# Optimization experiments

Measured on AMD Instinct MI355X. Metric: run time of the kernel, lower is better.

The kernel has to match this reference:

```python
import jax, jax.numpy as jnp
import numpy as np

N = 50000
E = 800000
F_IN = 128
F_HID = 128
F_OUT = 64


def setup_inputs() -> dict:
    key = jax.random.key(0)
    ks = jax.random.split(key, 16)
    x = jax.random.normal(ks[0], (N, F_IN), dtype=jnp.float32)
    ei1 = jax.random.randint(ks[1], (2, E), 0, N, dtype=jnp.int32)
    ei2 = jax.random.randint(ks[2], (2, E), 0, N, dtype=jnp.int32)
    ei3 = jax.random.randint(ks[3], (2, E), 0, N, dtype=jnp.int32)
    s = lambda k, i, o: jax.random.normal(k, (i, o), dtype=jnp.float32) / np.sqrt(i)
    Wl1 = s(ks[4], F_IN, F_HID); Wr1 = s(ks[5], F_IN, F_HID); b1 = jnp.zeros((F_HID,), jnp.float32)
    Wl2 = s(ks[6], F_HID, F_HID); Wr2 = s(ks[7], F_HID, F_HID); b2 = jnp.zeros((F_HID,), jnp.float32)
    Wl3 = s(ks[8], F_HID, F_OUT); Wr3 = s(ks[9], F_HID, F_OUT); b3 = jnp.zeros((F_OUT,), jnp.float32)
    return {"x": x, "ei1": ei1, "ei2": ei2, "ei3": ei3,
            "Wl1": Wl1, "Wr1": Wr1, "b1": b1,
            "Wl2": Wl2, "Wr2": Wr2, "b2": b2,
            "Wl3": Wl3, "Wr3": Wr3, "b3": b3}


def sage_conv(x, ei, Wl, Wr, b):
    # mean aggregation over incoming edges: src=ei[0] -> dst=ei[1]
    msg = x[ei[0]]                                            # [E, F]
    agg = jax.ops.segment_sum(msg, ei[1], num_segments=N)     # [N, F]
    cnt = jax.ops.segment_sum(jnp.ones((ei.shape[1],), x.dtype), ei[1], num_segments=N)
    mean = agg / jnp.maximum(cnt, 1.0)[:, None]
    # out = lin_l(mean) + lin_r(x_target); full-graph so x_target = x
    return mean @ Wl + b + x @ Wr


def reference(x, ei1, ei2, ei3, Wl1, Wr1, b1, Wl2, Wr2, b2, Wl3, Wr3, b3):
    # in_conv + relu (dropout is identity in eval mode)
    h = jax.nn.relu(sage_conv(x, ei1, Wl1, Wr1, b1))
    # mid_conv + relu + residual skip
    m = jax.nn.relu(sage_conv(h, ei2, Wl2, Wr2, b2))
    h = m + h
    # out_conv (no norm, no activation)
    return sage_conv(h, ei3, Wl3, Wr3, b3)
```

## Files before the change

kernel.cpp:

```cpp
#include <hip/hip_runtime.h>

#define FDIM 128
#define NBMAX 128
#define CAPB 10240

typedef short short8 __attribute__((ext_vector_type(8)));
typedef float f32x4 __attribute__((ext_vector_type(4)));

static __device__ __forceinline__ unsigned short f2bf(float f) {
    unsigned u = __float_as_uint(f);
    u += 0x7FFF + ((u >> 16) & 1);
    return (unsigned short)(u >> 16);
}
static __device__ __forceinline__ float bf2f(unsigned short h) {
    return __uint_as_float(((unsigned)h) << 16);
}

__global__ __launch_bounds__(256) void pack_kernel(
    int* __restrict__ gCnt, int nb3,
    const float* __restrict__ Wl1, const float* __restrict__ Wr1,
    const float* __restrict__ Wl2, const float* __restrict__ Wr2,
    const float* __restrict__ Wl3, const float* __restrict__ Wr3,
    ushort* __restrict__ Wp1, ushort* __restrict__ Wp2, ushort* __restrict__ Wp3)
{
    int b = blockIdx.x;
    if (b == 0) {
        for (int k = threadIdx.x; k < nb3; k += 256) gCnt[k] = 0;
    }
    if (b < 32) {
        const float *Wl, *Wr; ushort* Wp; int base;
        if (b < 16) { Wl = Wl1; Wr = Wr1; Wp = Wp1; base = b; }
        else        { Wl = Wl2; Wr = Wr2; Wp = Wp2; base = b - 16; }
        int idx = base * 256 + threadIdx.x;
        int lane = idx & 63;
        int jt = (idx >> 6) % 8;
        int kt = (idx >> 6) / 8;
        int kbase = kt * 32 + (lane >> 4) * 8;
        int j = jt * 16 + (lane & 15);
        const float* W = (kbase < 128) ? Wl : Wr;
        int kb = kbase & 127;
        ushort tmp[8];
#pragma unroll
        for (int t = 0; t < 8; ++t) tmp[t] = f2bf(W[(size_t)(kb + t) * 128 + j]);
        *reinterpret_cast<uint4*>(Wp + (size_t)idx * 8) = *reinterpret_cast<uint4*>(tmp);
        return;
    }
    int idx = (b - 32) * 256 + threadIdx.x;
    if (idx >= 4 * 8 * 64) return;
    int lane = idx & 63;
    int jt = (idx >> 6) % 8;
    int kt = (idx >> 6) / 8;
    int kbase = kt * 32 + (lane >> 4) * 8;
    int j = jt * 16 + (lane & 15);
    const float* W = (j < 64) ? Wl3 : Wr3;
    int jj = j & 63;
    ushort tmp[8];
#pragma unroll
    for (int t = 0; t < 8; ++t) tmp[t] = f2bf(W[(size_t)(kbase + t) * 64 + jj]);
    *reinterpret_cast<uint4*>(Wp3 + (size_t)idx * 8) = *reinterpret_cast<uint4*>(tmp);
}

__global__ __launch_bounds__(256) void binconv_kernel(
    const int* __restrict__ ei1, const int* __restrict__ ei2, const int* __restrict__ ei3,
    int* __restrict__ gCnt, unsigned* __restrict__ binned,
    int E, int NB, int bpg,
    const float* __restrict__ x, ushort* __restrict__ xb, int n4)
{
    __shared__ int hist[NBMAX];
    __shared__ int excl[NBMAX];
    __shared__ int cursor[NBMAX];
    __shared__ int gbase[NBMAX];
    __shared__ unsigned stag[4096];

    const int nbin = 3 * bpg;
    if ((int)blockIdx.x >= nbin) {
        int i = (blockIdx.x - nbin) * 256 + threadIdx.x;
        if (i >= n4) return;
        float4 v = reinterpret_cast<const float4*>(x)[i];
        ushort4 o = { f2bf(v.x), f2bf(v.y), f2bf(v.z), f2bf(v.w) };
        reinterpret_cast<ushort4*>(xb)[i] = o;
        return;
    }
    const int g = blockIdx.x / bpg;
    const int c = blockIdx.x % bpg;
    const int* ei = (g == 0) ? ei1 : (g == 1) ? ei2 : ei3;
    const int e0 = c * 4096;
    const int chunk = min(4096, E - e0);
    const int t = threadIdx.x;

    if (t < NB) hist[t] = 0;
    __syncthreads();
    for (int i = t; i < chunk; i += 256)
        atomicAdd(&hist[ei[E + e0 + i] >> 9], 1);
    __syncthreads();
    if (t < 64) {
        int a = (2 * t     < NB) ? hist[2 * t]     : 0;
        int b = (2 * t + 1 < NB) ? hist[2 * t + 1] : 0;
        int s = a + b, incl = s;
#pragma unroll
        for (int d = 1; d < 64; d <<= 1) {
            int x2 = __shfl_up(incl, d);
            if (t >= d) incl += x2;
        }
        int ex = incl - s;
        if (2 * t     < NB) { excl[2 * t]     = ex;     cursor[2 * t]     = ex; }
        if (2 * t + 1 < NB) { excl[2 * t + 1] = ex + a; cursor[2 * t + 1] = ex + a; }
    }
    __syncthreads();
    if (t < NB) {
        int cnt = hist[t];
        gbase[t] = cnt ? atomicAdd(&gCnt[g * NB + t], cnt) : 0;
    }
    __syncthreads();
    for (int i = t; i < chunk; i += 256) {
        int src = ei[e0 + i];
        int dst = ei[E + e0 + i];
        int pl = atomicAdd(&cursor[dst >> 9], 1);
        stag[pl] = ((unsigned)dst << 16) | (unsigned)src;
    }
    __syncthreads();
    for (int i = t; i < chunk; i += 256) {
        unsigned u = stag[i];
        int bk = u >> 25;
        int off = gbase[bk] + (i - excl[bk]);
        if (off < CAPB)
            binned[(size_t)(g * NB + bk) * CAPB + off] = u;
    }
}

__global__ __launch_bounds__(256) void fill2_kernel(
    const unsigned* __restrict__ binned, const int* __restrict__ gCnt,
    int* __restrict__ rowptr, ushort* __restrict__ colu, int N, int NB)
{
    __shared__ int hist[512];
    __shared__ int cursor[512];
    __shared__ int wsum[4];
    __shared__ int sColBase, sTotal;

    const int M = 3 * NB;
    const int gb = blockIdx.x;
    const int g = gb / NB, b = gb % NB;
    const int t = threadIdx.x;
    const int lane = t & 63, w = t >> 6;

    {
        int v0 = (2 * t     < M) ? gCnt[2 * t]     : 0;
        int v1 = (2 * t + 1 < M) ? gCnt[2 * t + 1] : 0;
        int s2 = v0 + v1, incl = s2;
#pragma unroll
        for (int d = 1; d < 64; d <<= 1) {
            int x = __shfl_up(incl, d);
            if (lane >= d) incl += x;
        }
        if (lane == 63) wsum[w] = incl;
        __syncthreads();
        int woff = 0;
        for (int ww = 0; ww < w; ++ww) woff += wsum[ww];
        int ex = woff + incl - s2;
        if (2 * t     == gb) sColBase = ex;
        if (2 * t + 1 == gb) sColBase = ex + v0;
        if (2 * t     == M - 1) sTotal = ex + v0;
        if (2 * t + 1 == M - 1) sTotal = ex + v0 + v1;
        __syncthreads();
    }
    const int colBase = sColBase;
    if (gb == 0 && t == 0) rowptr[(size_t)3 * N] = sTotal;

    const int n0 = b << 9;
    const int NL = min(512, N - n0);
    const int cnt = min(gCnt[gb], CAPB);
    const size_t ebase = (size_t)gb * CAPB;

    __syncthreads();
    hist[t] = 0; hist[t + 256] = 0;
    __syncthreads();
    for (int e = t; e < cnt; e += 256)
        atomicAdd(&hist[(binned[ebase + e] >> 16) & 511], 1);
    __syncthreads();
    int a = hist[2 * t], bb = hist[2 * t + 1];
    int s2 = a + bb, incl = s2;
#pragma unroll
    for (int d = 1; d < 64; d <<= 1) {
        int x = __shfl_up(incl, d);
        if (lane >= d) incl += x;
    }
    if (lane == 63) wsum[w] = incl;
    __syncthreads();
    int woff = 0;
    for (int ww = 0; ww < w; ++ww) woff += wsum[ww];
    int ex = woff + incl - s2;
    if (2 * t     < NL) rowptr[(size_t)g * N + n0 + 2 * t]     = colBase + ex;
    if (2 * t + 1 < NL) rowptr[(size_t)g * N + n0 + 2 * t + 1] = colBase + ex + a;
    cursor[2 * t] = ex; cursor[2 * t + 1] = ex + a;
    __syncthreads();
    for (int e = t; e < cnt; e += 256) {
        unsigned u = binned[ebase + e];
        int pl = atomicAdd(&cursor[(u >> 16) & 511], 1);
        colu[colBase + pl] = (ushort)(u & 0xFFFFu);
    }
}

static __device__ __forceinline__ float4 unpk_lo(uint4 v) {
    return make_float4(__uint_as_float(v.x << 16), __uint_as_float(v.x & 0xFFFF0000u),
                       __uint_as_float(v.y << 16), __uint_as_float(v.y & 0xFFFF0000u));
}
static __device__ __forceinline__ float4 unpk_hi(uint4 v) {
    return make_float4(__uint_as_float(v.z << 16), __uint_as_float(v.z & 0xFFFF0000u),
                       __uint_as_float(v.w << 16), __uint_as_float(v.w & 0xFFFF0000u));
}

__global__ __launch_bounds__(256) void gather_kernel(
    const ushort* __restrict__ xb, const int* __restrict__ rp,
    const ushort* __restrict__ col, ushort* __restrict__ mb, int N)
{
    int node = blockIdx.x * 16 + (threadIdx.x >> 4);
    if (node >= N) return;
    int l = threadIdx.x & 15;
    int beg = rp[node], end = rp[node + 1];
    float4 a0 = make_float4(0.f, 0.f, 0.f, 0.f);
    float4 a1 = make_float4(0.f, 0.f, 0.f, 0.f);

    int e = beg;
    for (; e + 8 <= end; e += 8) {
        uint4 v0 = *reinterpret_cast<const uint4*>(xb + ((size_t)col[e]     << 7) + l * 8);
        uint4 v1 = *reinterpret_cast<const uint4*>(xb + ((size_t)col[e + 1] << 7) + l * 8);
        uint4 v2 = *reinterpret_cast<const uint4*>(xb + ((size_t)col[e + 2] << 7) + l * 8);
        uint4 v3 = *reinterpret_cast<const uint4*>(xb + ((size_t)col[e + 3] << 7) + l * 8);
        uint4 v4 = *reinterpret_cast<const uint4*>(xb + ((size_t)col[e + 4] << 7) + l * 8);
        uint4 v5 = *reinterpret_cast<const uint4*>(xb + ((size_t)col[e + 5] << 7) + l * 8);
        uint4 v6 = *reinterpret_cast<const uint4*>(xb + ((size_t)col[e + 6] << 7) + l * 8);
        uint4 v7 = *reinterpret_cast<const uint4*>(xb + ((size_t)col[e + 7] << 7) + l * 8);
        a0 += unpk_lo(v0); a1 += unpk_hi(v0);
        a0 += unpk_lo(v1); a1 += unpk_hi(v1);
        a0 += unpk_lo(v2); a1 += unpk_hi(v2);
        a0 += unpk_lo(v3); a1 += unpk_hi(v3);
        a0 += unpk_lo(v4); a1 += unpk_hi(v4);
        a0 += unpk_lo(v5); a1 += unpk_hi(v5);
        a0 += unpk_lo(v6); a1 += unpk_hi(v6);
        a0 += unpk_lo(v7); a1 += unpk_hi(v7);
    }
    if (e < end) {
        int last = end - 1;
        int c0 = col[e];
        int c1 = col[min(e + 1, last)];
        int c2 = col[min(e + 2, last)];
        int c3 = col[min(e + 3, last)];
        int c4 = col[min(e + 4, last)];
        int c5 = col[min(e + 5, last)];
        int c6 = col[min(e + 6, last)];
        int c7 = col[min(e + 7, last)];
        uint4 v0 = *reinterpret_cast<const uint4*>(xb + ((size_t)c0 << 7) + l * 8);
        uint4 v1 = *reinterpret_cast<const uint4*>(xb + ((size_t)c1 << 7) + l * 8);
        uint4 v2 = *reinterpret_cast<const uint4*>(xb + ((size_t)c2 << 7) + l * 8);
        uint4 v3 = *reinterpret_cast<const uint4*>(xb + ((size_t)c3 << 7) + l * 8);
        uint4 v4 = *reinterpret_cast<const uint4*>(xb + ((size_t)c4 << 7) + l * 8);
        uint4 v5 = *reinterpret_cast<const uint4*>(xb + ((size_t)c5 << 7) + l * 8);
        uint4 v6 = *reinterpret_cast<const uint4*>(xb + ((size_t)c6 << 7) + l * 8);
        uint4 v7 = *reinterpret_cast<const uint4*>(xb + ((size_t)c7 << 7) + l * 8);
        float m1 = (e + 1 <= last) ? 1.f : 0.f;
        float m2 = (e + 2 <= last) ? 1.f : 0.f;
        float m3 = (e + 3 <= last) ? 1.f : 0.f;
        float m4 = (e + 4 <= last) ? 1.f : 0.f;
        float m5 = (e + 5 <= last) ? 1.f : 0.f;
        float m6 = (e + 6 <= last) ? 1.f : 0.f;
        float m7 = (e + 7 <= last) ? 1.f : 0.f;
        a0 += unpk_lo(v0);      a1 += unpk_hi(v0);
        a0 += unpk_lo(v1) * m1; a1 += unpk_hi(v1) * m1;
        a0 += unpk_lo(v2) * m2; a1 += unpk_hi(v2) * m2;
        a0 += unpk_lo(v3) * m3; a1 += unpk_hi(v3) * m3;
        a0 += unpk_lo(v4) * m4; a1 += unpk_hi(v4) * m4;
        a0 += unpk_lo(v5) * m5; a1 += unpk_hi(v5) * m5;
        a0 += unpk_lo(v6) * m6; a1 += unpk_hi(v6) * m6;
        a0 += unpk_lo(v7) * m7; a1 += unpk_hi(v7) * m7;
    }

    int deg = end - beg;
    float inv = 1.0f / (float)(deg > 1 ? deg : 1);
    uint4 o;
    o.x = (unsigned)f2bf(a0.x * inv) | ((unsigned)f2bf(a0.y * inv) << 16);
    o.y = (unsigned)f2bf(a0.z * inv) | ((unsigned)f2bf(a0.w * inv) << 16);
    o.z = (unsigned)f2bf(a1.x * inv) | ((unsigned)f2bf(a1.y * inv) << 16);
    o.w = (unsigned)f2bf(a1.z * inv) | ((unsigned)f2bf(a1.w * inv) << 16);
    *reinterpret_cast<uint4*>(mb + ((size_t)node << 7) + l * 8) = o;
}

__global__ __launch_bounds__(256) void gather3_kernel(
    const ushort* __restrict__ y3, const int* __restrict__ rp,
    const ushort* __restrict__ col, float* __restrict__ out, int N)
{
    int node = blockIdx.x * 32 + (threadIdx.x >> 3);
    if (node >= N) return;
    int l = threadIdx.x & 7;
    int beg = rp[node], end = rp[node + 1];
    float4 a0 = make_float4(0.f, 0.f, 0.f, 0.f);
    float4 a1 = make_float4(0.f, 0.f, 0.f, 0.f);

    int e = beg;
    for (; e + 8 <= end; e += 8) {
        uint4 v0 = *reinterpret_cast<const uint4*>(y3 + ((size_t)col[e]     << 6) + l * 8);
        uint4 v1 = *reinterpret_cast<const uint4*>(y3 + ((size_t)col[e + 1] << 6) + l * 8);
        uint4 v2 = *reinterpret_cast<const uint4*>(y3 + ((size_t)col[e + 2] << 6) + l * 8);
        uint4 v3 = *reinterpret_cast<const uint4*>(y3 + ((size_t)col[e + 3] << 6) + l * 8);
        uint4 v4 = *reinterpret_cast<const uint4*>(y3 + ((size_t)col[e + 4] << 6) + l * 8);
        uint4 v5 = *reinterpret_cast<const uint4*>(y3 + ((size_t)col[e + 5] << 6) + l * 8);
        uint4 v6 = *reinterpret_cast<const uint4*>(y3 + ((size_t)col[e + 6] << 6) + l * 8);
        uint4 v7 = *reinterpret_cast<const uint4*>(y3 + ((size_t)col[e + 7] << 6) + l * 8);
        a0 += unpk_lo(v0); a1 += unpk_hi(v0);
        a0 += unpk_lo(v1); a1 += unpk_hi(v1);
        a0 += unpk_lo(v2); a1 += unpk_hi(v2);
        a0 += unpk_lo(v3); a1 += unpk_hi(v3);
        a0 += unpk_lo(v4); a1 += unpk_hi(v4);
        a0 += unpk_lo(v5); a1 += unpk_hi(v5);
        a0 += unpk_lo(v6); a1 += unpk_hi(v6);
        a0 += unpk_lo(v7); a1 += unpk_hi(v7);
    }
    if (e < end) {
        int last = end - 1;
        int c0 = col[e];
        int c1 = col[min(e + 1, last)];
        int c2 = col[min(e + 2, last)];
        int c3 = col[min(e + 3, last)];
        int c4 = col[min(e + 4, last)];
        int c5 = col[min(e + 5, last)];
        int c6 = col[min(e + 6, last)];
        int c7 = col[min(e + 7, last)];
        uint4 v0 = *reinterpret_cast<const uint4*>(y3 + ((size_t)c0 << 6) + l * 8);
        uint4 v1 = *reinterpret_cast<const uint4*>(y3 + ((size_t)c1 << 6) + l * 8);
        uint4 v2 = *reinterpret_cast<const uint4*>(y3 + ((size_t)c2 << 6) + l * 8);
        uint4 v3 = *reinterpret_cast<const uint4*>(y3 + ((size_t)c3 << 6) + l * 8);
        uint4 v4 = *reinterpret_cast<const uint4*>(y3 + ((size_t)c4 << 6) + l * 8);
        uint4 v5 = *reinterpret_cast<const uint4*>(y3 + ((size_t)c5 << 6) + l * 8);
        uint4 v6 = *reinterpret_cast<const uint4*>(y3 + ((size_t)c6 << 6) + l * 8);
        uint4 v7 = *reinterpret_cast<const uint4*>(y3 + ((size_t)c7 << 6) + l * 8);
        float m1 = (e + 1 <= last) ? 1.f : 0.f;
        float m2 = (e + 2 <= last) ? 1.f : 0.f;
        float m3 = (e + 3 <= last) ? 1.f : 0.f;
        float m4 = (e + 4 <= last) ? 1.f : 0.f;
        float m5 = (e + 5 <= last) ? 1.f : 0.f;
        float m6 = (e + 6 <= last) ? 1.f : 0.f;
        float m7 = (e + 7 <= last) ? 1.f : 0.f;
        a0 += unpk_lo(v0);      a1 += unpk_hi(v0);
        a0 += unpk_lo(v1) * m1; a1 += unpk_hi(v1) * m1;
        a0 += unpk_lo(v2) * m2; a1 += unpk_hi(v2) * m2;
        a0 += unpk_lo(v3) * m3; a1 += unpk_hi(v3) * m3;
        a0 += unpk_lo(v4) * m4; a1 += unpk_hi(v4) * m4;
        a0 += unpk_lo(v5) * m5; a1 += unpk_hi(v5) * m5;
        a0 += unpk_lo(v6) * m6; a1 += unpk_hi(v6) * m6;
        a0 += unpk_lo(v7) * m7; a1 += unpk_hi(v7) * m7;
    }

    int deg = end - beg;
    float inv = 1.0f / (float)(deg > 1 ? deg : 1);
    float* po = out + ((size_t)node << 6) + l * 8;
    float4 o0 = *reinterpret_cast<const float4*>(po);
    float4 o1 = *reinterpret_cast<const float4*>(po + 4);
    o0.x += a0.x * inv; o0.y += a0.y * inv; o0.z += a0.z * inv; o0.w += a0.w * inv;
    o1.x += a1.x * inv; o1.y += a1.y * inv; o1.z += a1.z * inv; o1.w += a1.w * inv;
    *reinterpret_cast<float4*>(po)     = o0;
    *reinterpret_cast<float4*>(po + 4) = o1;
}

__global__ __launch_bounds__(256) void mfma_gemm1(
    const ushort* __restrict__ mb, const ushort* __restrict__ xin,
    const ushort* __restrict__ Wp, const float* __restrict__ bias,
    ushort* __restrict__ outb, int N)
{
    __shared__ __align__(16) ushort sA[64 * 256];
    const int tid = threadIdx.x;
    const int n0 = blockIdx.x * 64;

    for (int idx = tid; idx < 64 * 32; idx += 256) {
        int r = idx >> 5, s = idx & 31;
        int n = n0 + r; if (n >= N) n = N - 1;
        const uint4* src = (s < 16)
            ? reinterpret_cast<const uint4*>(mb  + ((size_t)n << 7) + (s << 3))
            : reinterpret_cast<const uint4*>(xin + ((size_t)n << 7) + ((s - 16) << 3));
        int sp = (s & 24) | ((s ^ r) & 7);
        *reinterpret_cast<uint4*>(&sA[(r << 8) + (sp << 3)]) = *src;
    }
    __syncthreads();

    const int lane = tid & 63;
    const int w = tid >> 6;
    const int rloc = w * 16 + (lane & 15);
    const int q = lane >> 4;

    f32x4 acc[8];
#pragma unroll
    for (int jt = 0; jt < 8; ++jt) acc[jt] = (f32x4){0.f, 0.f, 0.f, 0.f};

#pragma unroll
    for (int kt = 0; kt < 8; ++kt) {
        int s = kt * 4 + q;
        int sp = (s & 24) | ((s ^ rloc) & 7);
        short8 a = *reinterpret_cast<const short8*>(&sA[(rloc << 8) + (sp << 3)]);
#pragma unroll
        for (int jt = 0; jt < 8; ++jt) {
            short8 b = *reinterpret_cast<const short8*>(Wp + ((size_t)((kt * 8 + jt) * 64 + lane) << 3));
            acc[jt] = __builtin_amdgcn_mfma_f32_16x16x32_bf16(a, b, acc[jt], 0, 0, 0);
        }
    }

#pragma unroll
    for (int jt = 0; jt < 8; ++jt) {
        int j = jt * 16 + (lane & 15);
        float bj = bias[j];
#pragma unroll
        for (int reg = 0; reg < 4; ++reg) {
            int n = n0 + w * 16 + q * 4 + reg;
            if (n < N)
                outb[((size_t)n << 7) + j] = f2bf(fmaxf(acc[jt][reg] + bj, 0.f));
        }
    }
}

__global__ __launch_bounds__(256) void mfma_gemm23(
    const ushort* __restrict__ mb, const ushort* __restrict__ hb,
    const ushort* __restrict__ Wp2, const float* __restrict__ b2,
    const ushort* __restrict__ Wp3, const float* __restrict__ b3,
    ushort* __restrict__ y3, float* __restrict__ out, int N)
{
    __shared__ __align__(16) ushort sA[64 * 256];
    const int tid = threadIdx.x;
    const int n0 = blockIdx.x * 64;

    for (int idx = tid; idx < 64 * 32; idx += 256) {
        int r = idx >> 5, s = idx & 31;
        int n = n0 + r; if (n >= N) n = N - 1;
        const uint4* src = (s < 16)
            ? reinterpret_cast<const uint4*>(mb + ((size_t)n << 7) + (s << 3))
            : reinterpret_cast<const uint4*>(hb + ((size_t)n << 7) + ((s - 16) << 3));
        int sp = (s & 24) | ((s ^ r) & 7);
        *reinterpret_cast<uint4*>(&sA[(r << 8) + (sp << 3)]) = *src;
    }
    __syncthreads();

    const int lane = tid & 63;
    const int w = tid >> 6;
    const int rloc = w * 16 + (lane & 15);
    const int q = lane >> 4;

    f32x4 acc[8];
#pragma unroll
    for (int jt = 0; jt < 8; ++jt) acc[jt] = (f32x4){0.f, 0.f, 0.f, 0.f};
#pragma unroll
    for (int kt = 0; kt < 8; ++kt) {
        int s = kt * 4 + q;
        int sp = (s & 24) | ((s ^ rloc) & 7);
        short8 a = *reinterpret_cast<const short8*>(&sA[(rloc << 8) + (sp << 3)]);
#pragma unroll
        for (int jt = 0; jt < 8; ++jt) {
            short8 b = *reinterpret_cast<const short8*>(Wp2 + ((size_t)((kt * 8 + jt) * 64 + lane) << 3));
            acc[jt] = __builtin_amdgcn_mfma_f32_16x16x32_bf16(a, b, acc[jt], 0, 0, 0);
        }
    }
    __syncthreads();

#pragma unroll
    for (int jt = 0; jt < 8; ++jt) {
        int j = jt * 16 + (lane & 15);
        float bj = b2[j];
        int s = j >> 3;
#pragma unroll
        for (int reg = 0; reg < 4; ++reg) {
            int r = w * 16 + q * 4 + reg;
            int n = n0 + r;
            float v = 0.f;
            if (n < N)
                v = fmaxf(acc[jt][reg] + bj, 0.f) + bf2f(hb[((size_t)n << 7) + j]);
            int sp = (s & 8) | ((s ^ r) & 7);
            sA[(r << 7) + (sp << 3) + (j & 7)] = f2bf(v);
        }
    }
    __syncthreads();

#pragma unroll
    for (int jt = 0; jt < 8; ++jt) acc[jt] = (f32x4){0.f, 0.f, 0.f, 0.f};
#pragma unroll
    for (int kt = 0; kt < 4; ++kt) {
        int s = kt * 4 + q;
        int sp = (s & 8) | ((s ^ rloc) & 7);
        short8 a = *reinterpret_cast<const short8*>(&sA[(rloc << 7) + (sp << 3)]);
#pragma unroll
        for (int jt = 0; jt < 8; ++jt) {
            short8 b = *reinterpret_cast<const short8*>(Wp3 + ((size_t)((kt * 8 + jt) * 64 + lane) << 3));
            acc[jt] = __builtin_amdgcn_mfma_f32_16x16x32_bf16(a, b, acc[jt], 0, 0, 0);
        }
    }

#pragma unroll
    for (int jt = 0; jt < 8; ++jt) {
        int j = jt * 16 + (lane & 15);
#pragma unroll
        for (int reg = 0; reg < 4; ++reg) {
            int n = n0 + w * 16 + q * 4 + reg;
            if (n < N) {
                if (jt < 4) {
                    y3[((size_t)n << 6) + j] = f2bf(acc[jt][reg]);
                } else {
                    out[((size_t)n << 6) + (j - 64)] = acc[jt][reg] + b3[j - 64];
                }
            }
        }
    }
}

extern "C" void kernel_launch(void* const* d_in, const int* in_sizes, int n_in,
                              void* d_out, int out_size, void* d_ws, size_t ws_size,
                              hipStream_t stream) {
    const float* x   = (const float*)d_in[0];
    const int*   ei1 = (const int*)d_in[1];
    const int*   ei2 = (const int*)d_in[2];
    const int*   ei3 = (const int*)d_in[3];
    const float* Wl1 = (const float*)d_in[4];
    const float* Wr1 = (const float*)d_in[5];
    const float* b1  = (const float*)d_in[6];
    const float* Wl2 = (const float*)d_in[7];
    const float* Wr2 = (const float*)d_in[8];
    const float* b2  = (const float*)d_in[9];
    const float* Wl3 = (const float*)d_in[10];
    const float* Wr3 = (const float*)d_in[11];
    const float* b3  = (const float*)d_in[12];
    float* out = (float*)d_out;

    const int N = in_sizes[0] / FDIM;
    const int E = in_sizes[1] / 2;
    const int NB = (N + 511) >> 9;

    auto al = [](size_t v) { return (v + 255) & ~(size_t)255; };
    char* ws = (char*)d_ws;
    ushort* xb   = (ushort*)ws;   ws += al((size_t)N * FDIM * 2);
    ushort* hb   = (ushort*)ws;   ws += al((size_t)N * FDIM * 2);
    ushort* mb   = (ushort*)ws;   ws += al((size_t)N * FDIM * 2);
    ushort* Wp1  = (ushort*)ws;   ws += al((size_t)8 * 8 * 64 * 8 * 2);
    ushort* Wp2  = (ushort*)ws;   ws += al((size_t)8 * 8 * 64 * 8 * 2);
    ushort* Wp3  = (ushort*)ws;   ws += al((size_t)4 * 8 * 64 * 8 * 2);
    int*     rowptr = (int*)ws;   ws += al((size_t)(3 * N + 1) * 4);
    int*     gCnt   = (int*)ws;   ws += al((size_t)(3 * NB) * 4);
    unsigned* binned = (unsigned*)ws; ws += al((size_t)3 * NB * CAPB * 4);
    ushort*  colu   = (ushort*)ws;

    const int bpg = (E + 4095) / 4096;
    const int n4  = N * FDIM / 4;
    const int gatherBlocks  = (N + 15) / 16;
    const int gather3Blocks = (N + 31) / 32;
    const int gemmBlocks    = (N + 63) / 64;

    pack_kernel<<<40, 256, 0, stream>>>(
        gCnt, 3 * NB, Wl1, Wr1, Wl2, Wr2, Wl3, Wr3, Wp1, Wp2, Wp3);

    binconv_kernel<<<3 * bpg + (n4 + 255) / 256, 256, 0, stream>>>(
        ei1, ei2, ei3, gCnt, binned, E, NB, bpg, x, xb, n4);

    fill2_kernel<<<3 * NB, 256, 0, stream>>>(binned, gCnt, rowptr, colu, N, NB);

    gather_kernel<<<gatherBlocks, 256, 0, stream>>>(xb, rowptr, colu, mb, N);
    mfma_gemm1<<<gemmBlocks, 256, 0, stream>>>(mb, xb, Wp1, b1, hb, N);

    gather_kernel<<<gatherBlocks, 256, 0, stream>>>(hb, rowptr + N, colu, mb, N);
    mfma_gemm23<<<gemmBlocks, 256, 0, stream>>>(mb, hb, Wp2, b2, Wp3, b3, mb, out, N);

    gather3_kernel<<<gather3Blocks, 256, 0, stream>>>(mb, rowptr + 2 * N, colu, out, N);
}
```

Before: 166.3 us.

## Fuse neighbor mean-gather into MFMA GEMM kernels per layer

Merges the gather/mean kernel with the following MFMA GEMM for layer 1 and for layers 2+3. Each block now builds a 16-node tile in shared memory, holding the aggregated mean and the self features, before running the MFMA. This drops the mb intermediate round trip through global memory and two kernel launches. In exchange, each block covers only 16 rows instead of 64, so every block reloads the full weight matrix from global or L2 memory. The GEMM phase may also stall while waiting on the irregular gather latency.

```diff
diff --git a/kernel.cpp b/kernel.cpp
--- a/kernel.cpp
+++ b/kernel.cpp
@@ -209,27 +209,23 @@
                        __uint_as_float(v.w << 16), __uint_as_float(v.w & 0xFFFF0000u));
 }
 
-__global__ __launch_bounds__(256) void gather_kernel(
-    const ushort* __restrict__ xb, const int* __restrict__ rp,
-    const ushort* __restrict__ col, ushort* __restrict__ mb, int N)
-{
-    int node = blockIdx.x * 16 + (threadIdx.x >> 4);
-    if (node >= N) return;
-    int l = threadIdx.x & 15;
-    int beg = rp[node], end = rp[node + 1];
+static __device__ __forceinline__ uint4 gather_mean(
+    const ushort* __restrict__ src, const int* __restrict__ rp,
+    const ushort* __restrict__ col, int n, int l)
+{
+    int beg = rp[n], end = rp[n + 1];
     float4 a0 = make_float4(0.f, 0.f, 0.f, 0.f);
     float4 a1 = make_float4(0.f, 0.f, 0.f, 0.f);
-
     int e = beg;
     for (; e + 8 <= end; e += 8) {
-        uint4 v0 = *reinterpret_cast<const uint4*>(xb + ((size_t)col[e]     << 7) + l * 8);
-        uint4 v1 = *reinterpret_cast<const uint4*>(xb + ((size_t)col[e + 1] << 7) + l * 8);
-        uint4 v2 = *reinterpret_cast<const uint4*>(xb + ((size_t)col[e + 2] << 7) + l * 8);
-        uint4 v3 = *reinterpret_cast<const uint4*>(xb + ((size_t)col[e + 3] << 7) + l * 8);
-        uint4 v4 = *reinterpret_cast<const uint4*>(xb + ((size_t)col[e + 4] << 7) + l * 8);
-        uint4 v5 = *reinterpret_cast<const uint4*>(xb + ((size_t)col[e + 5] << 7) + l * 8);
-        uint4 v6 = *reinterpret_cast<const uint4*>(xb + ((size_t)col[e + 6] << 7) + l * 8);
-        uint4 v7 = *reinterpret_cast<const uint4*>(xb + ((size_t)col[e + 7] << 7) + l * 8);
+        uint4 v0 = *reinterpret_cast<const uint4*>(src + ((size_t)col[e]     << 7) + l * 8);
+        uint4 v1 = *reinterpret_cast<const uint4*>(src + ((size_t)col[e + 1] << 7) + l * 8);
+        uint4 v2 = *reinterpret_cast<const uint4*>(src + ((size_t)col[e + 2] << 7) + l * 8);
+        uint4 v3 = *reinterpret_cast<const uint4*>(src + ((size_t)col[e + 3] << 7) + l * 8);
+        uint4 v4 = *reinterpret_cast<const uint4*>(src + ((size_t)col[e + 4] << 7) + l * 8);
+        uint4 v5 = *reinterpret_cast<const uint4*>(src + ((size_t)col[e + 5] << 7) + l * 8);
+        uint4 v6 = *reinterpret_cast<const uint4*>(src + ((size_t)col[e + 6] << 7) + l * 8);
+        uint4 v7 = *reinterpret_cast<const uint4*>(src + ((size_t)col[e + 7] << 7) + l * 8);
         a0 += unpk_lo(v0); a1 += unpk_hi(v0);
         a0 += unpk_lo(v1); a1 += unpk_hi(v1);
         a0 += unpk_lo(v2); a1 += unpk_hi(v2);
@@ -249,14 +245,14 @@
         int c5 = col[min(e + 5, last)];
         int c6 = col[min(e + 6, last)];
         int c7 = col[min(e + 7, last)];
-        uint4 v0 = *reinterpret_cast<const uint4*>(xb + ((size_t)c0 << 7) + l * 8);
-        uint4 v1 = *reinterpret_cast<const uint4*>(xb + ((size_t)c1 << 7) + l * 8);
-        uint4 v2 = *reinterpret_cast<const uint4*>(xb + ((size_t)c2 << 7) + l * 8);
-        uint4 v3 = *reinterpret_cast<const uint4*>(xb + ((size_t)c3 << 7) + l * 8);
-        uint4 v4 = *reinterpret_cast<const uint4*>(xb + ((size_t)c4 << 7) + l * 8);
-        uint4 v5 = *reinterpret_cast<const uint4*>(xb + ((size_t)c5 << 7) + l * 8);
-        uint4 v6 = *reinterpret_cast<const uint4*>(xb + ((size_t)c6 << 7) + l * 8);
-        uint4 v7 = *reinterpret_cast<const uint4*>(xb + ((size_t)c7 << 7) + l * 8);
+        uint4 v0 = *reinterpret_cast<const uint4*>(src + ((size_t)c0 << 7) + l * 8);
+        uint4 v1 = *reinterpret_cast<const uint4*>(src + ((size_t)c1 << 7) + l * 8);
+        uint4 v2 = *reinterpret_cast<const uint4*>(src + ((size_t)c2 << 7) + l * 8);
+        uint4 v3 = *reinterpret_cast<const uint4*>(src + ((size_t)c3 << 7) + l * 8);
+        uint4 v4 = *reinterpret_cast<const uint4*>(src + ((size_t)c4 << 7) + l * 8);
+        uint4 v5 = *reinterpret_cast<const uint4*>(src + ((size_t)c5 << 7) + l * 8);
+        uint4 v6 = *reinterpret_cast<const uint4*>(src + ((size_t)c6 << 7) + l * 8);
+        uint4 v7 = *reinterpret_cast<const uint4*>(src + ((size_t)c7 << 7) + l * 8);
         float m1 = (e + 1 <= last) ? 1.f : 0.f;
         float m2 = (e + 2 <= last) ? 1.f : 0.f;
         float m3 = (e + 3 <= last) ? 1.f : 0.f;
@@ -273,7 +269,6 @@
         a0 += unpk_lo(v6) * m6; a1 += unpk_hi(v6) * m6;
         a0 += unpk_lo(v7) * m7; a1 += unpk_hi(v7) * m7;
     }
-
     int deg = end - beg;
     float inv = 1.0f / (float)(deg > 1 ? deg : 1);
     uint4 o;
@@ -281,7 +276,166 @@
     o.y = (unsigned)f2bf(a0.z * inv) | ((unsigned)f2bf(a0.w * inv) << 16);
     o.z = (unsigned)f2bf(a1.x * inv) | ((unsigned)f2bf(a1.y * inv) << 16);
     o.w = (unsigned)f2bf(a1.z * inv) | ((unsigned)f2bf(a1.w * inv) << 16);
-    *reinterpret_cast<uint4*>(mb + ((size_t)node << 7) + l * 8) = o;
+    return o;
+}
+
+__global__ __launch_bounds__(256) void fused_l1(
+    const ushort* __restrict__ xb, const int* __restrict__ rp,
+    const ushort* __restrict__ col, const ushort* __restrict__ Wp,
+    const float* __restrict__ bias, ushort* __restrict__ hb, int N)
+{
+    __shared__ __align__(16) ushort sA[16 * 256];
+    const int tid = threadIdx.x;
+    const int grp = tid >> 4;
+    const int l = tid & 15;
+    const int n0 = blockIdx.x * 16;
+    int n = n0 + grp; if (n >= N) n = N - 1;
+
+    {
+        uint4 v = *reinterpret_cast<const uint4*>(xb + ((size_t)n << 7) + l * 8);
+        int s = 16 + l;
+        int sp = (s & 24) | ((s ^ grp) & 7);
+        *reinterpret_cast<uint4*>(&sA[(grp << 8) + (sp << 3)]) = v;
+    }
+    {
+        uint4 o = gather_mean(xb, rp, col, n, l);
+        int sp = (l & 24) | ((l ^ grp) & 7);
+        *reinterpret_cast<uint4*>(&sA[(grp << 8) + (sp << 3)]) = o;
+    }
+    __syncthreads();
+
+    const int lane = tid & 63;
+    const int w = tid >> 6;
+    const int rloc = lane & 15;
+    const int q = lane >> 4;
+
+    f32x4 acc[2];
+    acc[0] = (f32x4){0.f, 0.f, 0.f, 0.f};
+    acc[1] = (f32x4){0.f, 0.f, 0.f, 0.f};
+#pragma unroll
+    for (int kt = 0; kt < 8; ++kt) {
+        int s = kt * 4 + q;
+        int sp = (s & 24) | ((s ^ rloc) & 7);
+        short8 a = *reinterpret_cast<const short8*>(&sA[(rloc << 8) + (sp << 3)]);
+#pragma unroll
+        for (int jj = 0; jj < 2; ++jj) {
+            int jt = w * 2 + jj;
+            short8 b = *reinterpret_cast<const short8*>(Wp + ((size_t)((kt * 8 + jt) * 64 + lane) << 3));
+            acc[jj] = __builtin_amdgcn_mfma_f32_16x16x32_bf16(a, b, acc[jj], 0, 0, 0);
+        }
+    }
+
+#pragma unroll
+    for (int jj = 0; jj < 2; ++jj) {
+        int j = (w * 2 + jj) * 16 + (lane & 15);
+        float bj = bias[j];
+#pragma unroll
+        for (int reg = 0; reg < 4; ++reg) {
+            int nn = n0 + q * 4 + reg;
+            if (nn < N)
+                hb[((size_t)nn << 7) + j] = f2bf(fmaxf(acc[jj][reg] + bj, 0.f));
+        }
+    }
+}
+
+__global__ __launch_bounds__(256) void fused_l23(
+    const ushort* __restrict__ hb, const int* __restrict__ rp,
+    const ushort* __restrict__ col,
+    const ushort* __restrict__ Wp2, const float* __restrict__ b2,
+    const ushort* __restrict__ Wp3, const float* __restrict__ b3,
+    ushort* __restrict__ y3, float* __restrict__ out, int N)
+{
+    __shared__ __align__(16) ushort sA[16 * 256];
+    __shared__ __align__(16) ushort sH[16 * 128];
+    const int tid = threadIdx.x;
+    const int grp = tid >> 4;
+    const int l = tid & 15;
+    const int n0 = blockIdx.x * 16;
+    int n = n0 + grp; if (n >= N) n = N - 1;
+
+    {
+        uint4 v = *reinterpret_cast<const uint4*>(hb + ((size_t)n << 7) + l * 8);
+        int s = 16 + l;
+        int sp = (s & 24) | ((s ^ grp) & 7);
+        *reinterpret_cast<uint4*>(&sA[(grp << 8) + (sp << 3)]) = v;
+    }
+    {
+        uint4 o = gather_mean(hb, rp, col, n, l);
+        int sp = (l & 24) | ((l ^ grp) & 7);
+        *reinterpret_cast<uint4*>(&sA[(grp << 8) + (sp << 3)]) = o;
+    }
+    __syncthreads();
+
+    const int lane = tid & 63;
+    const int w = tid >> 6;
+    const int rloc = lane & 15;
+    const int q = lane >> 4;
+
+    f32x4 acc[2];
+    acc[0] = (f32x4){0.f, 0.f, 0.f, 0.f};
+    acc[1] = (f32x4){0.f, 0.f, 0.f, 0.f};
+#pragma unroll
+    for (int kt = 0; kt < 8; ++kt) {
+        int s = kt * 4 + q;
+        int sp = (s & 24) | ((s ^ rloc) & 7);
+        short8 a = *reinterpret_cast<const short8*>(&sA[(rloc << 8) + (sp << 3)]);
+#pragma unroll
+        for (int jj = 0; jj < 2; ++jj) {
+            int jt = w * 2 + jj;
+            short8 b = *reinterpret_cast<const short8*>(Wp2 + ((size_t)((kt * 8 + jt) * 64 + lane) << 3));
+            acc[jj] = __builtin_amdgcn_mfma_f32_16x16x32_bf16(a, b, acc[jj], 0, 0, 0);
+        }
+    }
+
+#pragma unroll
+    for (int jj = 0; jj < 2; ++jj) {
+        int j = (w * 2 + jj) * 16 + (lane & 15);
+        float bj = b2[j];
+        int sSelf = 16 + (j >> 3);
+        int s = j >> 3;
+#pragma unroll
+        for (int reg = 0; reg < 4; ++reg) {
+            int r = q * 4 + reg;
+            int spSelf = (sSelf & 24) | ((sSelf ^ r) & 7);
+            float hself = bf2f(sA[(r << 8) + (spSelf << 3) + (j & 7)]);
+            float v = fmaxf(acc[jj][reg] + bj, 0.f) + hself;
+            int sp = (s & 8) | ((s ^ r) & 7);
+            sH[(r << 7) + (sp << 3) + (j & 7)] = f2bf(v);
+        }
+    }
+    __syncthreads();
+
+    acc[0] = (f32x4){0.f, 0.f, 0.f, 0.f};
+    acc[1] = (f32x4){0.f, 0.f, 0.f, 0.f};
+#pragma unroll
+    for (int kt = 0; kt < 4; ++kt) {
+        int s = kt * 4 + q;
+        int sp = (s & 8) | ((s ^ rloc) & 7);
+        short8 a = *reinterpret_cast<const short8*>(&sH[(rloc << 7) + (sp << 3)]);
+#pragma unroll
+        for (int jj = 0; jj < 2; ++jj) {
+            int jt = w * 2 + jj;
+            short8 b = *reinterpret_cast<const short8*>(Wp3 + ((size_t)((kt * 8 + jt) * 64 + lane) << 3));
+            acc[jj] = __builtin_amdgcn_mfma_f32_16x16x32_bf16(a, b, acc[jj], 0, 0, 0);
+        }
+    }
+
+#pragma unroll
+    for (int jj = 0; jj < 2; ++jj) {
+        int jt = w * 2 + jj;
+        int j = jt * 16 + (lane & 15);
+#pragma unroll
+        for (int reg = 0; reg < 4; ++reg) {
+            int nn = n0 + q * 4 + reg;
+            if (nn < N) {
+                if (jt < 4) {
+                    y3[((size_t)nn << 6) + j] = f2bf(acc[jj][reg]);
+                } else {
+                    out[((size_t)nn << 6) + (j - 64)] = acc[jj][reg] + b3[j - 64];
+                }
+            }
+        }
+    }
 }
 
 __global__ __launch_bounds__(256) void gather3_kernel(
@@ -360,151 +514,6 @@
     *reinterpret_cast<float4*>(po + 4) = o1;
 }
 
-__global__ __launch_bounds__(256) void mfma_gemm1(
-    const ushort* __restrict__ mb, const ushort* __restrict__ xin,
-    const ushort* __restrict__ Wp, const float* __restrict__ bias,
-    ushort* __restrict__ outb, int N)
-{
-    __shared__ __align__(16) ushort sA[64 * 256];
-    const int tid = threadIdx.x;
-    const int n0 = blockIdx.x * 64;
-
-    for (int idx = tid; idx < 64 * 32; idx += 256) {
-        int r = idx >> 5, s = idx & 31;
-        int n = n0 + r; if (n >= N) n = N - 1;
-        const uint4* src = (s < 16)
-            ? reinterpret_cast<const uint4*>(mb  + ((size_t)n << 7) + (s << 3))
-            : reinterpret_cast<const uint4*>(xin + ((size_t)n << 7) + ((s - 16) << 3));
-        int sp = (s & 24) | ((s ^ r) & 7);
-        *reinterpret_cast<uint4*>(&sA[(r << 8) + (sp << 3)]) = *src;
-    }
-    __syncthreads();
-
-    const int lane = tid & 63;
-    const int w = tid >> 6;
-    const int rloc = w * 16 + (lane & 15);
-    const int q = lane >> 4;
-
-    f32x4 acc[8];
-#pragma unroll
-    for (int jt = 0; jt < 8; ++jt) acc[jt] = (f32x4){0.f, 0.f, 0.f, 0.f};
-
-#pragma unroll
-    for (int kt = 0; kt < 8; ++kt) {
-        int s = kt * 4 + q;
-        int sp = (s & 24) | ((s ^ rloc) & 7);
-        short8 a = *reinterpret_cast<const short8*>(&sA[(rloc << 8) + (sp << 3)]);
-#pragma unroll
-        for (int jt = 0; jt < 8; ++jt) {
-            short8 b = *reinterpret_cast<const short8*>(Wp + ((size_t)((kt * 8 + jt) * 64 + lane) << 3));
-            acc[jt] = __builtin_amdgcn_mfma_f32_16x16x32_bf16(a, b, acc[jt], 0, 0, 0);
-        }
-    }
-
-#pragma unroll
-    for (int jt = 0; jt < 8; ++jt) {
-        int j = jt * 16 + (lane & 15);
-        float bj = bias[j];
-#pragma unroll
-        for (int reg = 0; reg < 4; ++reg) {
-            int n = n0 + w * 16 + q * 4 + reg;
-            if (n < N)
-                outb[((size_t)n << 7) + j] = f2bf(fmaxf(acc[jt][reg] + bj, 0.f));
-        }
-    }
-}
-
-__global__ __launch_bounds__(256) void mfma_gemm23(
-    const ushort* __restrict__ mb, const ushort* __restrict__ hb,
-    const ushort* __restrict__ Wp2, const float* __restrict__ b2,
-    const ushort* __restrict__ Wp3, const float* __restrict__ b3,
-    ushort* __restrict__ y3, float* __restrict__ out, int N)
-{
-    __shared__ __align__(16) ushort sA[64 * 256];
-    const int tid = threadIdx.x;
-    const int n0 = blockIdx.x * 64;
-
-    for (int idx = tid; idx < 64 * 32; idx += 256) {
-        int r = idx >> 5, s = idx & 31;
-        int n = n0 + r; if (n >= N) n = N - 1;
-        const uint4* src = (s < 16)
-            ? reinterpret_cast<const uint4*>(mb + ((size_t)n << 7) + (s << 3))
-            : reinterpret_cast<const uint4*>(hb + ((size_t)n << 7) + ((s - 16) << 3));
-        int sp = (s & 24) | ((s ^ r) & 7);
-        *reinterpret_cast<uint4*>(&sA[(r << 8) + (sp << 3)]) = *src;
-    }
-    __syncthreads();
-
-    const int lane = tid & 63;
-    const int w = tid >> 6;
-    const int rloc = w * 16 + (lane & 15);
-    const int q = lane >> 4;
-
-    f32x4 acc[8];
-#pragma unroll
-    for (int jt = 0; jt < 8; ++jt) acc[jt] = (f32x4){0.f, 0.f, 0.f, 0.f};
-#pragma unroll
-    for (int kt = 0; kt < 8; ++kt) {
-        int s = kt * 4 + q;
-        int sp = (s & 24) | ((s ^ rloc) & 7);
-        short8 a = *reinterpret_cast<const short8*>(&sA[(rloc << 8) + (sp << 3)]);
-#pragma unroll
-        for (int jt = 0; jt < 8; ++jt) {
-            short8 b = *reinterpret_cast<const short8*>(Wp2 + ((size_t)((kt * 8 + jt) * 64 + lane) << 3));
-            acc[jt] = __builtin_amdgcn_mfma_f32_16x16x32_bf16(a, b, acc[jt], 0, 0, 0);
-        }
-    }
-    __syncthreads();
-
-#pragma unroll
-    for (int jt = 0; jt < 8; ++jt) {
-        int j = jt * 16 + (lane & 15);
-        float bj = b2[j];
-        int s = j >> 3;
-#pragma unroll
-        for (int reg = 0; reg < 4; ++reg) {
-            int r = w * 16 + q * 4 + reg;
-            int n = n0 + r;
-            float v = 0.f;
-            if (n < N)
-                v = fmaxf(acc[jt][reg] + bj, 0.f) + bf2f(hb[((size_t)n << 7) + j]);
-            int sp = (s & 8) | ((s ^ r) & 7);
-            sA[(r << 7) + (sp << 3) + (j & 7)] = f2bf(v);
-        }
-    }
-    __syncthreads();
-
-#pragma unroll
-    for (int jt = 0; jt < 8; ++jt) acc[jt] = (f32x4){0.f, 0.f, 0.f, 0.f};
-#pragma unroll
-    for (int kt = 0; kt < 4; ++kt) {
-        int s = kt * 4 + q;
-        int sp = (s & 8) | ((s ^ rloc) & 7);
-        short8 a = *reinterpret_cast<const short8*>(&sA[(rloc << 7) + (sp << 3)]);
-#pragma unroll
-        for (int jt = 0; jt < 8; ++jt) {
-            short8 b = *reinterpret_cast<const short8*>(Wp3 + ((size_t)((kt * 8 + jt) * 64 + lane) << 3));
-            acc[jt] = __builtin_amdgcn_mfma_f32_16x16x32_bf16(a, b, acc[jt], 0, 0, 0);
-        }
-    }
-
-#pragma unroll
-    for (int jt = 0; jt < 8; ++jt) {
-        int j = jt * 16 + (lane & 15);
-#pragma unroll
-        for (int reg = 0; reg < 4; ++reg) {
-            int n = n0 + w * 16 + q * 4 + reg;
-            if (n < N) {
-                if (jt < 4) {
-                    y3[((size_t)n << 6) + j] = f2bf(acc[jt][reg]);
-                } else {
-                    out[((size_t)n << 6) + (j - 64)] = acc[jt][reg] + b3[j - 64];
-                }
-            }
-        }
-    }
-}
-
 extern "C" void kernel_launch(void* const* d_in, const int* in_sizes, int n_in,
                               void* d_out, int out_size, void* d_ws, size_t ws_size,
                               hipStream_t stream) {
@@ -531,7 +540,7 @@
     char* ws = (char*)d_ws;
     ushort* xb   = (ushort*)ws;   ws += al((size_t)N * FDIM * 2);
     ushort* hb   = (ushort*)ws;   ws += al((size_t)N * FDIM * 2);
-    ushort* mb   = (ushort*)ws;   ws += al((size_t)N * FDIM * 2);
+    ushort* y3   = (ushort*)ws;   ws += al((size_t)N * 64 * 2);
     ushort* Wp1  = (ushort*)ws;   ws += al((size_t)8 * 8 * 64 * 8 * 2);
     ushort* Wp2  = (ushort*)ws;   ws += al((size_t)8 * 8 * 64 * 8 * 2);
     ushort* Wp3  = (ushort*)ws;   ws += al((size_t)4 * 8 * 64 * 8 * 2);
@@ -542,9 +551,8 @@
 
     const int bpg = (E + 4095) / 4096;
     const int n4  = N * FDIM / 4;
-    const int gatherBlocks  = (N + 15) / 16;
+    const int fusedBlocks   = (N + 15) / 16;
     const int gather3Blocks = (N + 31) / 32;
-    const int gemmBlocks    = (N + 63) / 64;
 
     pack_kernel<<<40, 256, 0, stream>>>(
         gCnt, 3 * NB, Wl1, Wr1, Wl2, Wr2, Wl3, Wr3, Wp1, Wp2, Wp3);
@@ -554,11 +562,10 @@
 
     fill2_kernel<<<3 * NB, 256, 0, stream>>>(binned, gCnt, rowptr, colu, N, NB);
 
-    gather_kernel<<<gatherBlocks, 256, 0, stream>>>(xb, rowptr, colu, mb, N);
-    mfma_gemm1<<<gemmBlocks, 256, 0, stream>>>(mb, xb, Wp1, b1, hb, N);
-
-    gather_kernel<<<gatherBlocks, 256, 0, stream>>>(hb, rowptr + N, colu, mb, N);
-    mfma_gemm23<<<gemmBlocks, 256, 0, stream>>>(mb, hb, Wp2, b2, Wp3, b3, mb, out, N);
-
-    gather3_kernel<<<gather3Blocks, 256, 0, stream>>>(mb, rowptr + 2 * N, colu, out, N);
-}
+    fused_l1<<<fusedBlocks, 256, 0, stream>>>(xb, rowptr, colu, Wp1, b1, hb, N);
+
+    fused_l23<<<fusedBlocks, 256, 0, stream>>>(
+        hb, rowptr + N, colu, Wp2, b2, Wp3, b3, y3, out, N);
+
+    gather3_kernel<<<gather3Blocks, 256, 0, stream>>>(y3, rowptr + 2 * N, colu, out, N);
+}
```

Measured after the change: 145.6 us (median of 3 runs). 12.5% less time.
